# Performance work log

Hardware: AMD Instinct MI355X
Metric: run time of the kernel (lower is better)

## Reference

```python
import jax, jax.numpy as jnp
import numpy as np

D_MODEL = 2048
D_HEAD = 128
N_HEADS = D_MODEL // D_HEAD
SEQ_LENS = (512, 768, 384, 384)  # packed varlen sequences, sum = 2048
L_TOTAL = sum(SEQ_LENS)
EPS = 1e-6


def setup_inputs() -> dict:
    key = jax.random.key(0)
    ks = jax.random.split(key, 8)
    x = jax.random.normal(ks[0], (L_TOTAL, D_MODEL), jnp.float32)
    # Flux-style rope table: pairwise-duplicated cos/sin, pe = concat([cos, sin], -1) -> (L, 2*d_head)
    half = D_HEAD // 2
    pos = np.arange(L_TOTAL, dtype=np.float32)[:, None]
    freqs = 1.0 / (10000.0 ** (np.arange(half, dtype=np.float32) / half))  # (half,)
    ang = pos * freqs[None, :]                      # (L, half)
    cos = np.repeat(np.cos(ang), 2, axis=-1)        # (L, d_head), duplicated per pair
    sin = np.repeat(np.sin(ang), 2, axis=-1)
    pe = jnp.asarray(np.concatenate([cos, sin], axis=-1))  # (L, 2*d_head)
    seq_lens = jnp.asarray(SEQ_LENS, dtype=jnp.int32)
    std = 0.02
    qkv_w = std * jax.random.truncated_normal(ks[1], -2.0, 2.0, (3 * D_MODEL, D_MODEL), jnp.float32)
    qkv_b = jnp.zeros((3 * D_MODEL,), jnp.float32)
    q_scale = jnp.ones((D_HEAD,), jnp.float32)
    k_scale = jnp.ones((D_HEAD,), jnp.float32)
    proj_w = std * jax.random.truncated_normal(ks[2], -2.0, 2.0, (D_MODEL, D_MODEL), jnp.float32)
    proj_b = jnp.zeros((D_MODEL,), jnp.float32)
    return {"x": x, "pe": pe, "seq_lens": seq_lens, "qkv_w": qkv_w, "qkv_b": qkv_b,
            "q_scale": q_scale, "k_scale": k_scale, "proj_w": proj_w, "proj_b": proj_b}


def _rms_norm(t, scale):
    tf = t.astype(jnp.float32)
    rrms = jax.lax.rsqrt(jnp.mean(tf * tf, axis=-1, keepdims=True) + EPS)
    return (tf * rrms * scale).astype(t.dtype)


def _apply_rope(t, pe):
    # t: (L, nh, dh); pe: (L, 2*dh) with pairwise-duplicated cos|sin
    L, nh, dh = t.shape
    c = pe[:, None, 0:dh:2]     # (L, 1, dh/2) per-pair cos
    s = pe[:, None, dh::2]      # (L, 1, dh/2) per-pair sin
    tr = t.reshape(L, nh, dh // 2, 2)
    t1, t2 = tr[..., 0], tr[..., 1]
    out = jnp.stack([t1 * c - t2 * s, t1 * s + t2 * c], axis=-1)
    return out.reshape(L, nh, dh)


def reference(x, pe, seq_lens, qkv_w, qkv_b, q_scale, k_scale, proj_w, proj_b):
    L = x.shape[0]
    qkv = x @ qkv_w.T + qkv_b                      # (L, 3*D)
    q, k, v = jnp.split(qkv, 3, axis=-1)
    q = q.reshape(L, N_HEADS, D_HEAD)
    k = k.reshape(L, N_HEADS, D_HEAD)
    v = v.reshape(L, N_HEADS, D_HEAD)
    q = _rms_norm(q, q_scale)
    k = _rms_norm(k, k_scale)
    q = _apply_rope(q, pe)
    k = _apply_rope(k, pe)
    # block-diagonal (packed varlen) attention
    n = seq_lens.shape[0]
    seg = jnp.repeat(jnp.arange(n, dtype=jnp.int32), seq_lens, total_repeat_length=L)  # (L,)
    mask = seg[:, None] == seg[None, :]            # (L, L) block-diagonal
    scale = 1.0 / jnp.sqrt(jnp.float32(D_HEAD))
    scores = jnp.einsum('lhd,mhd->hlm', q, k) * scale  # (nh, L, L)
    scores = jnp.where(mask[None], scores, jnp.finfo(scores.dtype).min)
    p = jax.nn.softmax(scores, axis=-1)
    out = jnp.einsum('hlm,mhd->lhd', p, v)         # (L, nh, dh)
    out = out.reshape(L, D_MODEL)
    return out @ proj_w.T + proj_b
```

## Files before the change

kernel.cpp:

```cpp
#include <hip/hip_runtime.h>

typedef unsigned short ushort_t;
typedef __attribute__((ext_vector_type(4))) float f4;
typedef __attribute__((ext_vector_type(8))) short s8v;
typedef __attribute__((ext_vector_type(8))) __bf16 bf8v;

#define AS1 __attribute__((address_space(1)))
#define AS3 __attribute__((address_space(3)))

__device__ __forceinline__ void async16(void* lds, const void* g) {
    __builtin_amdgcn_global_load_lds((AS1 const void*)g, (AS3 void*)lds, 16, 0, 0);
}

__device__ __forceinline__ f4 mfma16(s8v a, s8v b, f4 c) {
    return __builtin_amdgcn_mfma_f32_16x16x32_bf16(
        __builtin_bit_cast(bf8v, a), __builtin_bit_cast(bf8v, b), c, 0, 0, 0);
}

__device__ __forceinline__ ushort_t f2bf(float f) {
    unsigned int u = __float_as_uint(f);
    u += 0x7fffu + ((u >> 16) & 1u);
    return (ushort_t)(u >> 16);
}
__device__ __forceinline__ float bf2f(ushort_t u) {
    return __uint_as_float(((unsigned int)u) << 16);
}

#define L_TOT   2048
#define DMODEL  2048
#define DHEAD   128
#define NHEADS  16

__global__ __launch_bounds__(256) void cast_all(const float* __restrict__ x,
                                                const float* __restrict__ w1,
                                                const float* __restrict__ w2,
                                                ushort_t* __restrict__ xo,
                                                ushort_t* __restrict__ w1o,
                                                ushort_t* __restrict__ w2o) {
    int i = blockIdx.x * 256 + threadIdx.x;
    const float* src; ushort_t* dst; int off;
    if (i < 1048576)      { src = x;  dst = xo;  off = 0; }
    else if (i < 4194304) { src = w1; dst = w1o; off = 1048576; }
    else                  { src = w2; dst = w2o; off = 4194304; }
    int j = i - off;
    float4 v = ((const float4*)src)[j];
    ushort4 o;
    o.x = f2bf(v.x); o.y = f2bf(v.y); o.z = f2bf(v.z); o.w = f2bf(v.w);
    ((ushort4*)dst)[j] = o;
}


__global__ __launch_bounds__(256) void gemm_qkv(const ushort_t* __restrict__ A,
                                                const ushort_t* __restrict__ Bt,
                                                const float* __restrict__ bias,
                                                ushort_t* __restrict__ qk_out,
                                                ushort_t* __restrict__ vt_out,
                                                int K) {
    __shared__ alignas(16) ushort_t sA[128 * 64];
    __shared__ alignas(16) ushort_t sB[128 * 64];

    const int tid  = threadIdx.x;
    const int lane = tid & 63;
    const int wave = tid >> 6;
    const int wr = (wave >> 1) * 64;
    const int wc = (wave & 1) * 64;
    const int bm = blockIdx.x * 128;
    const int bn = blockIdx.y * 128;
    const bool is_v = blockIdx.y >= 32;

    f4 acc[4][4];
#pragma unroll
    for (int i = 0; i < 4; i++)
#pragma unroll
        for (int j = 0; j < 4; j++) acc[i][j] = (f4){0.f, 0.f, 0.f, 0.f};

    const int rs  = tid >> 3;
    const int csw = ((tid & 7) ^ (rs & 7)) * 8;
    const ushort_t* Abase = A  + (size_t)(bm + rs) * K + csw;
    const ushort_t* Bbase = Bt + (size_t)(bn + rs) * K + csw;

    const ushort_t* fA = is_v ? sB : sA;
    const ushort_t* fB = is_v ? sA : sB;
    const int arow = wr + (lane & 15);
    const int brow = wc + (lane & 15);
    const int l7 = lane & 7;
    const int o0 = (((lane >> 4)    ) ^ l7) * 8;
    const int o1 = (((lane >> 4) + 4) ^ l7) * 8;

    for (int k0 = 0; k0 < K; k0 += 64) {
#pragma unroll
        for (int s = 0; s < 4; s++) {
            async16(&sA[tid * 8 + s * 2048], Abase + k0 + (size_t)(32 * s) * K);
            async16(&sB[tid * 8 + s * 2048], Bbase + k0 + (size_t)(32 * s) * K);
        }
        __syncthreads();

        s8v af[4], bfr[4];
#pragma unroll
        for (int i = 0; i < 4; i++) af[i]  = *(const s8v*)&fA[(arow + i * 16) * 64 + o0];
#pragma unroll
        for (int j = 0; j < 4; j++) bfr[j] = *(const s8v*)&fB[(brow + j * 16) * 64 + o0];
#pragma unroll
        for (int i = 0; i < 4; i++)
#pragma unroll
            for (int j = 0; j < 4; j++) acc[i][j] = mfma16(af[i], bfr[j], acc[i][j]);

#pragma unroll
        for (int i = 0; i < 4; i++) af[i]  = *(const s8v*)&fA[(arow + i * 16) * 64 + o1];
#pragma unroll
        for (int j = 0; j < 4; j++) bfr[j] = *(const s8v*)&fB[(brow + j * 16) * 64 + o1];
#pragma unroll
        for (int i = 0; i < 4; i++)
#pragma unroll
            for (int j = 0; j < 4; j++) acc[i][j] = mfma16(af[i], bfr[j], acc[i][j]);
        __syncthreads();
    }

    const int q = lane & 15;
    const int g = lane >> 4;

    if (!is_v) {
        const int crow0 = bm + wr + g * 4;
        const int ccol0 = bn + wc + q;
#pragma unroll
        for (int j = 0; j < 4; j++) {
            int col = ccol0 + j * 16;
            float bv = bias[col];
#pragma unroll
            for (int i = 0; i < 4; i++) {
                int r0 = crow0 + i * 16;
#pragma unroll
                for (int r = 0; r < 4; r++)
                    qk_out[(size_t)(r0 + r) * 4096 + col] = f2bf(acc[i][j][r] + bv);
            }
        }
    } else {
        const int c0   = (blockIdx.y - 32) * 128 + wr + g * 4;
        const int tok0 = bm + wc + q;
#pragma unroll
        for (int i = 0; i < 4; i++) {
#pragma unroll
            for (int r = 0; r < 4; r++) {
                int c = c0 + i * 16 + r;
                float bv = bias[4096 + c];
#pragma unroll
                for (int j = 0; j < 4; j++)
                    vt_out[(size_t)c * L_TOT + tok0 + j * 16] = f2bf(acc[i][j][r] + bv);
            }
        }
    }
}

__global__ __launch_bounds__(256) void gemm_proj(const ushort_t* __restrict__ A,
                                                 const ushort_t* __restrict__ Bt,
                                                 float* __restrict__ Cf,
                                                 int K) {
    __shared__ alignas(16) ushort_t sA[128 * 64];
    __shared__ alignas(16) ushort_t sB[128 * 64];
    const int tid  = threadIdx.x;
    const int lane = tid & 63;
    const int wave = tid >> 6;
    const int wr = (wave >> 1) * 64;
    const int wc = (wave & 1) * 64;
    const int bm = blockIdx.x * 128;
    const int bn = blockIdx.y * 128;

    f4 acc[4][4];
#pragma unroll
    for (int i = 0; i < 4; i++)
#pragma unroll
        for (int j = 0; j < 4; j++) acc[i][j] = (f4){0.f, 0.f, 0.f, 0.f};

    const int rs  = tid >> 3;
    const int csw = ((tid & 7) ^ (rs & 7)) * 8;
    const ushort_t* Abase = A  + (size_t)(bm + rs) * K + csw;
    const ushort_t* Bbase = Bt + (size_t)(bn + rs) * K + csw;
    const int arow = wr + (lane & 15);
    const int brow = wc + (lane & 15);
    const int l7 = lane & 7;
    const int o0 = (((lane >> 4)    ) ^ l7) * 8;
    const int o1 = (((lane >> 4) + 4) ^ l7) * 8;
    const int kbeg = blockIdx.z * (K >> 1);
    const int kend = kbeg + (K >> 1);

    for (int k0 = kbeg; k0 < kend; k0 += 64) {
#pragma unroll
        for (int s = 0; s < 4; s++) {
            async16(&sA[tid * 8 + s * 2048], Abase + k0 + (size_t)(32 * s) * K);
            async16(&sB[tid * 8 + s * 2048], Bbase + k0 + (size_t)(32 * s) * K);
        }
        __syncthreads();

        s8v af[4], bfr[4];
#pragma unroll
        for (int i = 0; i < 4; i++) af[i]  = *(const s8v*)&sA[(arow + i * 16) * 64 + o0];
#pragma unroll
        for (int j = 0; j < 4; j++) bfr[j] = *(const s8v*)&sB[(brow + j * 16) * 64 + o0];
#pragma unroll
        for (int i = 0; i < 4; i++)
#pragma unroll
            for (int j = 0; j < 4; j++) acc[i][j] = mfma16(af[i], bfr[j], acc[i][j]);

#pragma unroll
        for (int i = 0; i < 4; i++) af[i]  = *(const s8v*)&sA[(arow + i * 16) * 64 + o1];
#pragma unroll
        for (int j = 0; j < 4; j++) bfr[j] = *(const s8v*)&sB[(brow + j * 16) * 64 + o1];
#pragma unroll
        for (int i = 0; i < 4; i++)
#pragma unroll
            for (int j = 0; j < 4; j++) acc[i][j] = mfma16(af[i], bfr[j], acc[i][j]);
        __syncthreads();
    }

    const int q = lane & 15;
    const int g = lane >> 4;
    const int crow0 = bm + wr + g * 4;
    const int ccol0 = bn + wc + q;
    float* Cp = Cf + (size_t)blockIdx.z * L_TOT * DMODEL;
#pragma unroll
    for (int j = 0; j < 4; j++) {
        int col = ccol0 + j * 16;
#pragma unroll
        for (int i = 0; i < 4; i++) {
#pragma unroll
            for (int r = 0; r < 4; r++)
                Cp[(size_t)(crow0 + i * 16 + r) * DMODEL + col] = acc[i][j][r];
        }
    }
}

__global__ __launch_bounds__(256) void reduce_bias(const float* __restrict__ part,
                                                   const float* __restrict__ bias,
                                                   float* __restrict__ out) {
    int i = blockIdx.x * 256 + threadIdx.x;
    f4 a = ((const f4*)part)[i];
    f4 b = ((const f4*)(part + (size_t)L_TOT * DMODEL))[i];
    f4 bv = ((const f4*)bias)[i & 511];
    ((f4*)out)[i] = a + b + bv;
}

__global__ __launch_bounds__(256) void norm_rope(const ushort_t* __restrict__ qk,
                                                 const float* __restrict__ pe,
                                                 const float* __restrict__ q_scale,
                                                 const float* __restrict__ k_scale,
                                                 ushort_t* __restrict__ qh,
                                                 ushort_t* __restrict__ kh) {
    int wid  = blockIdx.x * 4 + (threadIdx.x >> 6);
    int lane = threadIdx.x & 63;
    int l = wid >> 4;
    int h = wid & 15;

    const ushort_t* base = qk + (size_t)l * 4096 + h * DHEAD + 2 * lane;
    ushort2 qu = *(const ushort2*)base;
    ushort2 ku = *(const ushort2*)(base + 2048);
    float qvx = bf2f(qu.x), qvy = bf2f(qu.y);
    float kvx = bf2f(ku.x), kvy = bf2f(ku.y);

    float qss = qvx * qvx + qvy * qvy;
    float kss = kvx * kvx + kvy * kvy;
#pragma unroll
    for (int m = 32; m >= 1; m >>= 1) {
        qss += __shfl_xor(qss, m);
        kss += __shfl_xor(kss, m);
    }
    float qr = rsqrtf(qss * (1.0f / DHEAD) + 1e-6f);
    float kr = rsqrtf(kss * (1.0f / DHEAD) + 1e-6f);

    float c = pe[(size_t)l * 256 + 2 * lane];
    float s = pe[(size_t)l * 256 + 128 + 2 * lane];

    float q1 = qvx * qr * q_scale[2 * lane];
    float q2 = qvy * qr * q_scale[2 * lane + 1];
    float k1 = kvx * kr * k_scale[2 * lane];
    float k2 = kvy * kr * k_scale[2 * lane + 1];

    const float sc = 0.08838834764831845f;
    float qo0 = (q1 * c - q2 * s) * sc;
    float qo1 = (q1 * s + q2 * c) * sc;
    float ko0 = k1 * c - k2 * s;
    float ko1 = k1 * s + k2 * c;

    size_t o = ((size_t)h * L_TOT + l) * DHEAD + 2 * lane;
    ushort2 qp, kp;
    qp.x = f2bf(qo0); qp.y = f2bf(qo1);
    kp.x = f2bf(ko0); kp.y = f2bf(ko1);
    *(ushort2*)(qh + o) = qp;
    *(ushort2*)(kh + o) = kp;
}

__global__ __launch_bounds__(256) void attn_kernel(const ushort_t* __restrict__ qh,
                                                   const ushort_t* __restrict__ kh,
                                                   const ushort_t* __restrict__ vt,
                                                   ushort_t* __restrict__ attn_out) {
    __shared__ alignas(16) ushort_t sK[64 * 128];
    __shared__ alignas(16) ushort_t sV[128 * 64];
    __shared__ alignas(16) ushort_t sP[4][16 * 64];

    const int qt = blockIdx.x;
    const int h  = blockIdx.y;
    const int tid = threadIdx.x;
    const int lane = tid & 63;
    const int w = tid >> 6;
    const int qrow0 = qt * 64 + w * 16;

    int q0 = qt * 64;
    int seg_start, seg_end;
    if (q0 < 512)       { seg_start = 0;    seg_end = 512;  }
    else if (q0 < 1280) { seg_start = 512;  seg_end = 1280; }
    else if (q0 < 1664) { seg_start = 1280; seg_end = 1664; }
    else                { seg_start = 1664; seg_end = 2048; }

    const int g = lane >> 4;
    const int q = lane & 15;
    const int qa7 = q & 7;

    const ushort_t* ksrc[4];
    const ushort_t* vsrc[4];
#pragma unroll
    for (int i = 0; i < 4; i++) {
        int p = i * 256 + tid;
        ksrc[i] = kh + ((size_t)h * L_TOT + (p >> 4)) * DHEAD + ((p & 15) ^ ((p >> 4) & 7)) * 8;
        vsrc[i] = vt + ((size_t)h * DHEAD + (p >> 3)) * L_TOT + ((p & 7) ^ ((p >> 3) & 7)) * 8;
    }

    s8v qf[4];
    {
        const ushort_t* qbase = qh + ((size_t)h * L_TOT + qrow0 + q) * DHEAD;
#pragma unroll
        for (int kd = 0; kd < 4; kd++) qf[kd] = *(const s8v*)(qbase + kd * 32 + g * 8);
    }

    f4 o[8];
#pragma unroll
    for (int j = 0; j < 8; j++) o[j] = (f4){0.f, 0.f, 0.f, 0.f};
    float lsum[4] = {0.f, 0.f, 0.f, 0.f};

    for (int kt = seg_start; kt < seg_end; kt += 64) {
#pragma unroll
        for (int i = 0; i < 4; i++) {
            int p = i * 256 + tid;
            async16(&sK[p * 8], ksrc[i] + (size_t)kt * DHEAD);
            async16(&sV[p * 8], vsrc[i] + kt);
        }
        __syncthreads();

        f4 S[4];
#pragma unroll
        for (int tj = 0; tj < 4; tj++) {
            f4 st = (f4){0.f, 0.f, 0.f, 0.f};
#pragma unroll
            for (int kd = 0; kd < 4; kd++) {
                s8v bfrag = *(const s8v*)&sK[(tj * 16 + q) * 128 + (((kd * 4 + g) ^ qa7) * 8)];
                st = mfma16(qf[kd], bfrag, st);
            }
            S[tj] = st;
        }

#pragma unroll
        for (int tj = 0; tj < 4; tj++)
#pragma unroll
            for (int r = 0; r < 4; r++) {
                float p = __expf(S[tj][r]);
                S[tj][r] = p;
                lsum[r] += p;
            }

#pragma unroll
        for (int tj = 0; tj < 4; tj++) {
            int cg = tj * 2 + (q >> 3);
#pragma unroll
            for (int r = 0; r < 4; r++) {
                int prow = g * 4 + r;
                sP[w][prow * 64 + ((cg ^ (prow & 7)) * 8) + qa7] = f2bf(S[tj][r]);
            }
        }
        asm volatile("s_waitcnt lgkmcnt(0)" ::: "memory");

#pragma unroll
        for (int ks = 0; ks < 2; ks++) {
            s8v pf = *(const s8v*)&sP[w][q * 64 + (((ks * 4 + g) ^ qa7) * 8)];
#pragma unroll
            for (int j = 0; j < 8; j++) {
                s8v vf = *(const s8v*)&sV[(j * 16 + q) * 64 + (((ks * 4 + g) ^ qa7) * 8)];
                o[j] = mfma16(pf, vf, o[j]);
            }
        }
        __syncthreads();
    }

#pragma unroll
    for (int r = 0; r < 4; r++) {
        float rs = lsum[r];
        rs += __shfl_xor(rs, 1);
        rs += __shfl_xor(rs, 2);
        rs += __shfl_xor(rs, 4);
        rs += __shfl_xor(rs, 8);
        int row = qrow0 + g * 4 + r;
        float inv = 1.0f / rs;
#pragma unroll
        for (int j = 0; j < 8; j++) {
            attn_out[(size_t)row * DMODEL + h * DHEAD + j * 16 + q] = f2bf(o[j][r] * inv);
        }
    }
}

extern "C" void kernel_launch(void* const* d_in, const int* in_sizes, int n_in,
                              void* d_out, int out_size, void* d_ws, size_t ws_size,
                              hipStream_t stream) {
    const float* x       = (const float*)d_in[0];
    const float* pe      = (const float*)d_in[1];
    const float* qkv_w   = (const float*)d_in[3];
    const float* qkv_b   = (const float*)d_in[4];
    const float* q_scale = (const float*)d_in[5];
    const float* k_scale = (const float*)d_in[6];
    const float* proj_w  = (const float*)d_in[7];
    const float* proj_b  = (const float*)d_in[8];
    float* out = (float*)d_out;

    char* ws = (char*)d_ws;
    const size_t MB = 1024 * 1024;
    ushort_t* x_bf     = (ushort_t*)(ws + 0);
    ushort_t* wqkv_bf  = (ushort_t*)(ws + 8 * MB);
    ushort_t* wproj_bf = (ushort_t*)(ws + 32 * MB);
    ushort_t* qk_bf    = (ushort_t*)(ws + 40 * MB);
    ushort_t* qh       = (ushort_t*)(ws + 57 * MB);
    ushort_t* kh       = (ushort_t*)(ws + 65 * MB);
    ushort_t* vt       = (ushort_t*)(ws + 73 * MB);
    ushort_t* attn_b   = (ushort_t*)(ws + 81 * MB);
    float*    part     = (float*)   (ws + 40 * MB);

    cast_all<<<20480, 256, 0, stream>>>(x, qkv_w, proj_w, x_bf, wqkv_bf, wproj_bf);

    gemm_qkv<<<dim3(16, 48), 256, 0, stream>>>(x_bf, wqkv_bf, qkv_b, qk_bf, vt, 2048);

    norm_rope<<<8192, 256, 0, stream>>>(qk_bf, pe, q_scale, k_scale, qh, kh);

    attn_kernel<<<dim3(32, 16), 256, 0, stream>>>(qh, kh, vt, attn_b);

    gemm_proj<<<dim3(16, 16, 2), 256, 0, stream>>>(attn_b, wproj_bf, part, 2048);
    reduce_bias<<<4096, 256, 0, stream>>>(part, proj_b, out);
}
```

Measured before the change: 284.5 us.

## Rewrite QKV GEMM as 256x256 tile, 8-wave, double-buffered pipelined kernel

Replaces the 128x128, 4-wave QKV GEMM with a 256x256 tile kernel using 8 waves and double-buffered LDS. Async global-to-LDS loads for the next K tiles are interleaved with MFMA clusters under fine-grained barriers, explicit vmcnt waits and setprio. This is meant to hide global load latency and raise data reuse per tile. In exchange it uses more LDS (128 KB per block) and launches fewer blocks (192), which may hurt occupancy and leave CUs idle.

```diff
diff --git a/kernel.cpp b/kernel.cpp
--- a/kernel.cpp
+++ b/kernel.cpp
@@ -50,102 +50,157 @@
 }
 
 
-__global__ __launch_bounds__(256) void gemm_qkv(const ushort_t* __restrict__ A,
-                                                const ushort_t* __restrict__ Bt,
-                                                const float* __restrict__ bias,
-                                                ushort_t* __restrict__ qk_out,
-                                                ushort_t* __restrict__ vt_out,
-                                                int K) {
-    __shared__ alignas(16) ushort_t sA[128 * 64];
-    __shared__ alignas(16) ushort_t sB[128 * 64];
+template <int P>
+__device__ __forceinline__ void cluster(f4 (&acc)[8][4], const s8v (&af)[2][2],
+                                        const s8v (&bf)[4][2]) {
+    __builtin_amdgcn_s_setprio(1);
+#pragma unroll
+    for (int mm = 0; mm < 2; mm++)
+#pragma unroll
+        for (int nn = 0; nn < 4; nn++) {
+            acc[2 * P + mm][nn] = mfma16(af[mm][0], bf[nn][0], acc[2 * P + mm][nn]);
+            acc[2 * P + mm][nn] = mfma16(af[mm][1], bf[nn][1], acc[2 * P + mm][nn]);
+        }
+    __builtin_amdgcn_s_setprio(0);
+}
+
+#define LDF(base, row, oo) (*(const s8v*)&(base)[(row) * 64 + (oo)])
+
+#define STG(dst, gb, Tt, h)                                                              \
+    async16(&(dst)[tid * 8 + (2 * (h)) * 4096],                                          \
+            (gb) + (size_t)(Tt) * 64 + (size_t)(128 * (h)) * K);                         \
+    async16(&(dst)[tid * 8 + (2 * (h) + 1) * 4096],                                      \
+            (gb) + (size_t)(Tt) * 64 + (size_t)(128 * (h) + 64) * K);
+
+#define TILE(cur, T)                                                                     \
+    {                                                                                    \
+        const int Tn1 = ((T) + 1 < NT) ? (T) + 1 : NT - 1;                               \
+        const int Tn2 = ((T) + 2 < NT) ? (T) + 2 : NT - 1;                               \
+        const ushort_t* fA = stA[cur];                                                   \
+        const ushort_t* fB = stB[cur];                                                   \
+        s8v bfrag[4][2];                                                                 \
+        s8v afrag[2][2];                                                                 \
+                                                                  \
+        bfrag[0][0] = LDF(fB, brow + 0,  o0); bfrag[0][1] = LDF(fB, brow + 0,  o1);      \
+        bfrag[1][0] = LDF(fB, brow + 16, o0); bfrag[1][1] = LDF(fB, brow + 16, o1);      \
+        bfrag[2][0] = LDF(fB, brow + 32, o0); bfrag[2][1] = LDF(fB, brow + 32, o1);      \
+        bfrag[3][0] = LDF(fB, brow + 48, o0); bfrag[3][1] = LDF(fB, brow + 48, o1);      \
+        afrag[0][0] = LDF(fA, arow + 0,  o0); afrag[0][1] = LDF(fA, arow + 0,  o1);      \
+        afrag[1][0] = LDF(fA, arow + 16, o0); afrag[1][1] = LDF(fA, arow + 16, o1);      \
+        STG(stA[(cur) ^ 1], gA, Tn1, 0)                                                  \
+        __builtin_amdgcn_s_barrier();                                                    \
+        cluster<0>(acc, afrag, bfrag);                                                   \
+        __builtin_amdgcn_s_barrier();                                                    \
+                                                                  \
+        afrag[0][0] = LDF(fA, arow + 32, o0); afrag[0][1] = LDF(fA, arow + 32, o1);      \
+        afrag[1][0] = LDF(fA, arow + 48, o0); afrag[1][1] = LDF(fA, arow + 48, o1);      \
+        STG(stA[(cur) ^ 1], gA, Tn1, 1)                                                  \
+        __builtin_amdgcn_s_barrier();                                                    \
+        cluster<1>(acc, afrag, bfrag);                                                   \
+        __builtin_amdgcn_s_barrier();                                                    \
+                                                                  \
+        afrag[0][0] = LDF(fA, arow + 64, o0); afrag[0][1] = LDF(fA, arow + 64, o1);      \
+        afrag[1][0] = LDF(fA, arow + 80, o0); afrag[1][1] = LDF(fA, arow + 80, o1);      \
+        STG(stB[cur], gB, Tn2, 0)                                                        \
+        __builtin_amdgcn_s_barrier();                                                    \
+        cluster<2>(acc, afrag, bfrag);                                                   \
+        __builtin_amdgcn_s_barrier();                                                    \
+                                                                  \
+        afrag[0][0] = LDF(fA, arow + 96,  o0); afrag[0][1] = LDF(fA, arow + 96,  o1);    \
+        afrag[1][0] = LDF(fA, arow + 112, o0); afrag[1][1] = LDF(fA, arow + 112, o1);    \
+        STG(stB[cur], gB, Tn2, 1)                                                        \
+        asm volatile("s_waitcnt vmcnt(4)" ::: "memory");                                 \
+        __builtin_amdgcn_sched_barrier(0);                                               \
+        __builtin_amdgcn_s_barrier();                                                    \
+        cluster<3>(acc, afrag, bfrag);                                                   \
+        __builtin_amdgcn_s_barrier();                                                    \
+    }
+
+__global__ __launch_bounds__(512, 2) void gemm_qkv256(const ushort_t* __restrict__ A,
+                                                      const ushort_t* __restrict__ Bt,
+                                                      const float* __restrict__ bias,
+                                                      ushort_t* __restrict__ qk_out,
+                                                      ushort_t* __restrict__ vt_out,
+                                                      int K) {
+    __shared__ alignas(16) ushort_t sA[2][16384];
+    __shared__ alignas(16) ushort_t sB[2][16384];
 
     const int tid  = threadIdx.x;
     const int lane = tid & 63;
     const int wave = tid >> 6;
-    const int wr = (wave >> 1) * 64;
-    const int wc = (wave & 1) * 64;
-    const int bm = blockIdx.x * 128;
-    const int bn = blockIdx.y * 128;
-    const bool is_v = blockIdx.y >= 32;
-
-    f4 acc[4][4];
-#pragma unroll
-    for (int i = 0; i < 4; i++)
-#pragma unroll
-        for (int j = 0; j < 4; j++) acc[i][j] = (f4){0.f, 0.f, 0.f, 0.f};
+    const int wm = wave >> 2;
+    const int wn = wave & 3;
+    const int bm = blockIdx.x * 256;
+    const int bn = blockIdx.y * 256;
+    const bool is_v = blockIdx.y >= 16;
+    const int NT = K >> 6;
+
+    const int q15 = lane & 15;
+    const int g   = lane >> 4;
+    const int l7  = lane & 7;
+    const int o0  = ((g    ) ^ l7) * 8;
+    const int o1  = ((g + 4) ^ l7) * 8;
+    const int arow = wm * 128 + q15;
+    const int brow = wn * 64 + q15;
 
     const int rs  = tid >> 3;
     const int csw = ((tid & 7) ^ (rs & 7)) * 8;
     const ushort_t* Abase = A  + (size_t)(bm + rs) * K + csw;
     const ushort_t* Bbase = Bt + (size_t)(bn + rs) * K + csw;
 
-    const ushort_t* fA = is_v ? sB : sA;
-    const ushort_t* fB = is_v ? sA : sB;
-    const int arow = wr + (lane & 15);
-    const int brow = wc + (lane & 15);
-    const int l7 = lane & 7;
-    const int o0 = (((lane >> 4)    ) ^ l7) * 8;
-    const int o1 = (((lane >> 4) + 4) ^ l7) * 8;
-
-    for (int k0 = 0; k0 < K; k0 += 64) {
-#pragma unroll
-        for (int s = 0; s < 4; s++) {
-            async16(&sA[tid * 8 + s * 2048], Abase + k0 + (size_t)(32 * s) * K);
-            async16(&sB[tid * 8 + s * 2048], Bbase + k0 + (size_t)(32 * s) * K);
-        }
-        __syncthreads();
-
-        s8v af[4], bfr[4];
-#pragma unroll
-        for (int i = 0; i < 4; i++) af[i]  = *(const s8v*)&fA[(arow + i * 16) * 64 + o0];
-#pragma unroll
-        for (int j = 0; j < 4; j++) bfr[j] = *(const s8v*)&fB[(brow + j * 16) * 64 + o0];
-#pragma unroll
-        for (int i = 0; i < 4; i++)
-#pragma unroll
-            for (int j = 0; j < 4; j++) acc[i][j] = mfma16(af[i], bfr[j], acc[i][j]);
-
-#pragma unroll
-        for (int i = 0; i < 4; i++) af[i]  = *(const s8v*)&fA[(arow + i * 16) * 64 + o1];
-#pragma unroll
-        for (int j = 0; j < 4; j++) bfr[j] = *(const s8v*)&fB[(brow + j * 16) * 64 + o1];
-#pragma unroll
-        for (int i = 0; i < 4; i++)
-#pragma unroll
-            for (int j = 0; j < 4; j++) acc[i][j] = mfma16(af[i], bfr[j], acc[i][j]);
-        __syncthreads();
-    }
-
-    const int q = lane & 15;
-    const int g = lane >> 4;
+    ushort_t* stA[2]; ushort_t* stB[2];
+    const ushort_t* gA; const ushort_t* gB;
+    if (!is_v) { stA[0] = sA[0]; stA[1] = sA[1]; stB[0] = sB[0]; stB[1] = sB[1];
+                 gA = Abase; gB = Bbase; }
+    else       { stA[0] = sB[0]; stA[1] = sB[1]; stB[0] = sA[0]; stB[1] = sA[1];
+                 gA = Bbase; gB = Abase; }
+
+    f4 acc[8][4];
+#pragma unroll
+    for (int i = 0; i < 8; i++)
+#pragma unroll
+        for (int j = 0; j < 4; j++) acc[i][j] = (f4){0.f, 0.f, 0.f, 0.f};
+
+    STG(stA[0], gA, 0, 0) STG(stA[0], gA, 0, 1)
+    STG(stB[0], gB, 0, 0) STG(stB[0], gB, 0, 1)
+    {
+        const int T1 = NT > 1 ? 1 : 0;
+        STG(stB[1], gB, T1, 0) STG(stB[1], gB, T1, 1)
+    }
+    asm volatile("s_waitcnt vmcnt(4)" ::: "memory");
+    __builtin_amdgcn_sched_barrier(0);
+    __builtin_amdgcn_s_barrier();
+
+    for (int T = 0; T < NT; T += 2) {
+        TILE(0, T)
+        TILE(1, T + 1)
+    }
 
     if (!is_v) {
-        const int crow0 = bm + wr + g * 4;
-        const int ccol0 = bn + wc + q;
-#pragma unroll
-        for (int j = 0; j < 4; j++) {
-            int col = ccol0 + j * 16;
+#pragma unroll
+        for (int n = 0; n < 4; n++) {
+            int col = bn + wn * 64 + n * 16 + q15;
             float bv = bias[col];
 #pragma unroll
-            for (int i = 0; i < 4; i++) {
-                int r0 = crow0 + i * 16;
+            for (int m = 0; m < 8; m++) {
+                int r0 = bm + wm * 128 + m * 16 + g * 4;
 #pragma unroll
                 for (int r = 0; r < 4; r++)
-                    qk_out[(size_t)(r0 + r) * 4096 + col] = f2bf(acc[i][j][r] + bv);
+                    qk_out[(size_t)(r0 + r) * 4096 + col] = f2bf(acc[m][n][r] + bv);
             }
         }
     } else {
-        const int c0   = (blockIdx.y - 32) * 128 + wr + g * 4;
-        const int tok0 = bm + wc + q;
-#pragma unroll
-        for (int i = 0; i < 4; i++) {
+        const int cb   = (blockIdx.y - 16) * 256 + wm * 128;
+        const int tok0 = bm + wn * 64 + q15;
+#pragma unroll
+        for (int m = 0; m < 8; m++) {
 #pragma unroll
             for (int r = 0; r < 4; r++) {
-                int c = c0 + i * 16 + r;
+                int c = cb + m * 16 + g * 4 + r;
                 float bv = bias[4096 + c];
 #pragma unroll
-                for (int j = 0; j < 4; j++)
-                    vt_out[(size_t)c * L_TOT + tok0 + j * 16] = f2bf(acc[i][j][r] + bv);
+                for (int n = 0; n < 4; n++)
+                    vt_out[(size_t)c * L_TOT + tok0 + n * 16] = f2bf(acc[m][n][r] + bv);
             }
         }
     }
@@ -155,8 +210,8 @@
                                                  const ushort_t* __restrict__ Bt,
                                                  float* __restrict__ Cf,
                                                  int K) {
-    __shared__ alignas(16) ushort_t sA[128 * 64];
-    __shared__ alignas(16) ushort_t sB[128 * 64];
+    __shared__ alignas(16) ushort_t pA[128 * 64];
+    __shared__ alignas(16) ushort_t pB[128 * 64];
     const int tid  = threadIdx.x;
     const int lane = tid & 63;
     const int wave = tid >> 6;
@@ -186,25 +241,25 @@
     for (int k0 = kbeg; k0 < kend; k0 += 64) {
 #pragma unroll
         for (int s = 0; s < 4; s++) {
-            async16(&sA[tid * 8 + s * 2048], Abase + k0 + (size_t)(32 * s) * K);
-            async16(&sB[tid * 8 + s * 2048], Bbase + k0 + (size_t)(32 * s) * K);
+            async16(&pA[tid * 8 + s * 2048], Abase + k0 + (size_t)(32 * s) * K);
+            async16(&pB[tid * 8 + s * 2048], Bbase + k0 + (size_t)(32 * s) * K);
         }
         __syncthreads();
 
         s8v af[4], bfr[4];
 #pragma unroll
-        for (int i = 0; i < 4; i++) af[i]  = *(const s8v*)&sA[(arow + i * 16) * 64 + o0];
-#pragma unroll
-        for (int j = 0; j < 4; j++) bfr[j] = *(const s8v*)&sB[(brow + j * 16) * 64 + o0];
+        for (int i = 0; i < 4; i++) af[i]  = *(const s8v*)&pA[(arow + i * 16) * 64 + o0];
+#pragma unroll
+        for (int j = 0; j < 4; j++) bfr[j] = *(const s8v*)&pB[(brow + j * 16) * 64 + o0];
 #pragma unroll
         for (int i = 0; i < 4; i++)
 #pragma unroll
             for (int j = 0; j < 4; j++) acc[i][j] = mfma16(af[i], bfr[j], acc[i][j]);
 
 #pragma unroll
-        for (int i = 0; i < 4; i++) af[i]  = *(const s8v*)&sA[(arow + i * 16) * 64 + o1];
-#pragma unroll
-        for (int j = 0; j < 4; j++) bfr[j] = *(const s8v*)&sB[(brow + j * 16) * 64 + o1];
+        for (int i = 0; i < 4; i++) af[i]  = *(const s8v*)&pA[(arow + i * 16) * 64 + o1];
+#pragma unroll
+        for (int j = 0; j < 4; j++) bfr[j] = *(const s8v*)&pB[(brow + j * 16) * 64 + o1];
 #pragma unroll
         for (int i = 0; i < 4; i++)
 #pragma unroll
@@ -431,7 +486,7 @@
 
     cast_all<<<20480, 256, 0, stream>>>(x, qkv_w, proj_w, x_bf, wqkv_bf, wproj_bf);
 
-    gemm_qkv<<<dim3(16, 48), 256, 0, stream>>>(x_bf, wqkv_bf, qkv_b, qk_bf, vt, 2048);
+    gemm_qkv256<<<dim3(8, 24), 512, 0, stream>>>(x_bf, wqkv_bf, qkv_b, qk_bf, vt, 2048);
 
     norm_rope<<<8192, 256, 0, stream>>>(qk_bf, pe, q_scale, k_scale, qh, kh);
 
```

Result: faster. 260.9 us (-8.3%).
